# Kernel tuning notes

Hardware: AMD Instinct MI355X
Metric: run time of the kernel (lower is better)

The kernel has to match this reference:

```python
import jax, jax.numpy as jnp
import numpy as np

B, S, E, H, L, D = 16, 512, 512, 8, 3, 64
OBS, ACT, NA = 128, 16, 8
KAPPAS = jnp.asarray(1.0 - 2.0 ** (-5.0 - np.arange(H)), jnp.float32)  # per-head retention decay, decay_scaling_factor=1.0
INV_SQRT_D = 1.0 / float(np.sqrt(D))


def rmsnorm(x, w, eps=1e-6):
    return x * jax.lax.rsqrt(jnp.mean(x * x, -1, keepdims=True) + eps) * w


def swiglu(x, wg, wp):
    return jax.nn.silu(x @ wg) * (x @ wp)


def sin_pe(ts, dim):
    # sinusoidal timestep positional encoding, ts: (B,S) float -> (B,S,dim)
    half = dim // 2
    freqs = jnp.exp(-np.log(10000.0) * jnp.arange(half, dtype=jnp.float32) / half)
    ang = ts[..., None] * freqs
    return jnp.concatenate([jnp.sin(ang), jnp.cos(ang)], -1)


def retention(xk, xq, xv, h0, ts, wq, wk, wv, wo, masked):
    # chunkwise multi-scale retention with cross-chunk recurrent state h0: (B,H,D,D)
    b, s, e = xq.shape
    pe = sin_pe(ts, e)
    q = ((xq + pe) @ wq).reshape(b, s, H, D).transpose(0, 2, 1, 3)            # (B,H,S,D)
    k = ((xk + pe) @ wk).reshape(b, s, H, D).transpose(0, 2, 1, 3) * INV_SQRT_D
    v = ((xv + pe) @ wv).reshape(b, s, H, D).transpose(0, 2, 1, 3)
    lk = jnp.log(KAPPAS)                                                      # (H,)
    diff = ts[:, None, :, None] - ts[:, None, None, :]                        # (B,1,S,S) timestep gaps
    if masked:
        idx = jnp.arange(s)
        allow = (diff > 0) | ((diff == 0) & (idx[:, None] >= idx[None, :]))
        dmat = jnp.where(allow, jnp.exp(lk[None, :, None, None] * diff), 0.0)
    else:
        dmat = jnp.exp(lk[None, :, None, None] * jnp.abs(diff))
    scores = jnp.einsum('bhnd,bhmd->bhnm', q, k) * dmat                       # decay-masked scores
    xi = jnp.exp(lk[None, :, None] * (ts[:, None, :] + 1.0))                  # (B,H,S) cross-chunk decay
    out = jnp.einsum('bhnm,bhmd->bhnd', scores, v) + jnp.einsum('bhnd,bhde->bhne', q, h0) * xi[..., None]
    tmax = ts.max(-1)                                                         # (B,)
    wst = jnp.exp(lk[None, :, None] * (tmax[:, None, None] - ts[:, None, :]))  # (B,H,S)
    h_new = jnp.exp(lk[None, :] * (tmax[:, None] + 1.0))[..., None, None] * h0 \
        + jnp.einsum('bhm,bhmd,bhme->bhde', wst, k, v)
    out = out.transpose(0, 2, 1, 3).reshape(b, s, e) @ wo
    return out, h_new


def _forward(obs, action, enc_hs, dec_hs1, dec_hs2, step_count, params):
    (eoln, eow, eln, ewq, ewk, ewv, ewo, eln1, eln2, efg, efp,
     ehw1, ehb1, ehln, ehw2, ehb2,
     daw, dln, dwq1, dwk1, dwv1, dwo1, dwq2, dwk2, dwv2, dwo2,
     dln1, dln2, dln3, dfg, dfp,
     dhw1, dhb1, dhln, dhw2, dhb2) = params
    ts = step_count.astype(jnp.float32)
    # ---- Encoder ----
    obs_rep = jax.nn.gelu(rmsnorm(obs, eoln) @ eow)
    enc_new = []
    for i in range(L):
        x = rmsnorm(obs_rep, eln)
        ret, hn = retention(x, x, x, enc_hs[:, i], ts, ewq[i], ewk[i], ewv[i], ewo[i], masked=False)
        x = rmsnorm(x + ret, eln1[i])
        obs_rep = rmsnorm(x + swiglu(x, efg[i], efp[i]), eln2[i])
        enc_new.append(hn)
    value = rmsnorm(jax.nn.gelu(obs_rep @ ehw1 + ehb1), ehln) @ ehw2 + ehb2
    # ---- Decoder ----
    x = rmsnorm(jax.nn.gelu(action @ daw), dln)
    d1_new, d2_new = [], []
    for i in range(L):
        ret, h1 = retention(x, x, x, dec_hs1[:, i], ts, dwq1[i], dwk1[i], dwv1[i], dwo1[i], masked=True)
        r = rmsnorm(x + ret, dln1[i])
        ret2, h2 = retention(r, obs_rep, r, dec_hs2[:, i], ts, dwq2[i], dwk2[i], dwv2[i], dwo2[i], masked=True)
        y = rmsnorm(obs_rep + ret2, dln2[i])
        x = rmsnorm(y + swiglu(y, dfg[i], dfp[i]), dln3[i])
        d1_new.append(h1)
        d2_new.append(h2)
    logits = rmsnorm(jax.nn.gelu(x @ dhw1 + dhb1), dhln) @ dhw2 + dhb2
    return value, logits, jnp.stack(enc_new, 1), jnp.stack(d1_new, 1), jnp.stack(d2_new, 1)


def setup_inputs():
    key = jax.random.key(0)
    ki = iter(jax.random.split(key, 50))
    def w(shape, s=0.02):
        return jax.random.normal(next(ki), shape, jnp.float32) * s
    inp = {
        'obs': jax.random.normal(next(ki), (B, S, OBS), jnp.float32),
        'action': jax.random.uniform(next(ki), (B, S, ACT + 1), jnp.float32),
        'enc_hs': jnp.zeros((B, L, H, D, D), jnp.float32),
        'dec_hs1': jnp.zeros((B, L, H, D, D), jnp.float32),
        'dec_hs2': jnp.zeros((B, L, H, D, D), jnp.float32),
        'step_count': jnp.broadcast_to(jnp.arange(S, dtype=jnp.int32) // NA, (B, S)),
        'enc_obs_ln_w': jnp.ones((OBS,), jnp.float32),
        'enc_obs_w': w((OBS, E)),
        'enc_ln_w': jnp.ones((E,), jnp.float32),
        'enc_wq': w((L, E, E)), 'enc_wk': w((L, E, E)), 'enc_wv': w((L, E, E)), 'enc_wo': w((L, E, E)),
        'enc_ln1_w': jnp.ones((L, E), jnp.float32), 'enc_ln2_w': jnp.ones((L, E), jnp.float32),
        'enc_ffn_gate': w((L, E, E)), 'enc_ffn_proj': w((L, E, E)),
        'enc_head_w1': w((E, E)), 'enc_head_b1': jnp.zeros((E,), jnp.float32),
        'enc_head_ln': jnp.ones((E,), jnp.float32),
        'enc_head_w2': w((E, 1)), 'enc_head_b2': jnp.zeros((1,), jnp.float32),
        'dec_act_w': w((ACT + 1, E)), 'dec_ln_w': jnp.ones((E,), jnp.float32),
        'dec_wq1': w((L, E, E)), 'dec_wk1': w((L, E, E)), 'dec_wv1': w((L, E, E)), 'dec_wo1': w((L, E, E)),
        'dec_wq2': w((L, E, E)), 'dec_wk2': w((L, E, E)), 'dec_wv2': w((L, E, E)), 'dec_wo2': w((L, E, E)),
        'dec_ln1_w': jnp.ones((L, E), jnp.float32), 'dec_ln2_w': jnp.ones((L, E), jnp.float32),
        'dec_ln3_w': jnp.ones((L, E), jnp.float32),
        'dec_ffn_gate': w((L, E, E)), 'dec_ffn_proj': w((L, E, E)),
        'dec_head_w1': w((E, E)), 'dec_head_b1': jnp.zeros((E,), jnp.float32),
        'dec_head_ln': jnp.ones((E,), jnp.float32),
        'dec_head_w2': w((E, ACT)), 'dec_head_b2': jnp.zeros((ACT,), jnp.float32),
    }
    return inp


def reference(obs, action, enc_hs, dec_hs1, dec_hs2, step_count, enc_obs_ln_w, enc_obs_w, enc_ln_w, enc_wq, enc_wk, enc_wv, enc_wo, enc_ln1_w, enc_ln2_w, enc_ffn_gate, enc_ffn_proj, enc_head_w1, enc_head_b1, enc_head_ln, enc_head_w2, enc_head_b2, dec_act_w, dec_ln_w, dec_wq1, dec_wk1, dec_wv1, dec_wo1, dec_wq2, dec_wk2, dec_wv2, dec_wo2, dec_ln1_w, dec_ln2_w, dec_ln3_w, dec_ffn_gate, dec_ffn_proj, dec_head_w1, dec_head_b1, dec_head_ln, dec_head_w2, dec_head_b2):
    params = (enc_obs_ln_w, enc_obs_w, enc_ln_w, enc_wq, enc_wk, enc_wv, enc_wo, enc_ln1_w, enc_ln2_w, enc_ffn_gate, enc_ffn_proj, enc_head_w1, enc_head_b1, enc_head_ln, enc_head_w2, enc_head_b2, dec_act_w, dec_ln_w, dec_wq1, dec_wk1, dec_wv1, dec_wo1, dec_wq2, dec_wk2, dec_wv2, dec_wo2, dec_ln1_w, dec_ln2_w, dec_ln3_w, dec_ffn_gate, dec_ffn_proj, dec_head_w1, dec_head_b1, dec_head_ln, dec_head_w2, dec_head_b2)
    return _forward(obs, action, enc_hs, dec_hs1, dec_hs2, step_count, params)
```

## Files before the change

### kernel.cpp

```cpp
#include <hip/hip_runtime.h>
#include <hip/hip_bf16.h>
#include <math.h>

typedef __attribute__((ext_vector_type(8))) short short8;
typedef __attribute__((ext_vector_type(4))) short short4v;
typedef __attribute__((ext_vector_type(4))) float f32x4;

#define BB 16
#define SS 512
#define EE 512
#define HH 8
#define DH 64
#define LL 3
#define MM (BB*SS)
#define OBSD 128
#define ACTD 17
#define INV_SQRT_D 0.125f

#define ACT_NONE 0
#define ACT_GELU 1

#define NORM_PLAIN 0
#define NORM_ADD 1

// ... 17 lines not shown
__device__ __forceinline__ void gl16(const void* g, void* l){
  __builtin_amdgcn_global_load_lds((gas1_t)g, (las3_t)l, 16, 0, 0);
}

#define PIPE_SYNC do{ asm volatile("s_waitcnt vmcnt(0)" ::: "memory"); \
                      __builtin_amdgcn_s_barrier(); \
                      __builtin_amdgcn_sched_barrier(0); }while(0)

__global__ __launch_bounds__(256) void wtpose_kernel(
    const float* __restrict__ src, unsigned short* __restrict__ dst, int K, int Kpad)
{
  __shared__ float t[32][33];
  const int gx = blockIdx.x, gy = blockIdx.y;
  const int tx = threadIdx.x, ty = threadIdx.y;
  #pragma unroll
  for (int i = 0; i < 4; ++i){
    int k = gx*32 + ty + i*8, n = gy*32 + tx;
    t[ty+i*8][tx] = (k < K) ? src[(size_t)k*EE + n] : 0.f;
  }
  __syncthreads();
  #pragma unroll
  for (int i = 0; i < 4; ++i){
    int k = gx*32 + tx, n = gy*32 + ty + i*8;
    dst[(size_t)n*Kpad + k] = f2bs(t[tx][ty+i*8]);
  }
}

struct TP50 { const float* s[50]; unsigned short* d[50]; };
__global__ __launch_bounds__(256) void wtpose_batch_kernel(TP50 tp)
{
  __shared__ float t[32][33];
  const float* src = tp.s[blockIdx.z];
  unsigned short* dst = tp.d[blockIdx.z];
  const int gx = blockIdx.x, gy = blockIdx.y;
  const int tx = threadIdx.x, ty = threadIdx.y;
  #pragma unroll
  for (int i = 0; i < 4; ++i){
    int k = gx*32 + ty + i*8, n = gy*32 + tx;
    t[ty+i*8][tx] = src[(size_t)k*EE + n];
  }
  __syncthreads();
  #pragma unroll
  for (int i = 0; i < 4; ++i){
    int k = gx*32 + tx, n = gy*32 + ty + i*8;
    dst[(size_t)n*EE + k] = f2bs(t[tx][ty+i*8]);
  }
}

template<int MODE>
__global__ __launch_bounds__(256) void gemm128_kernel(
    const unsigned short* __restrict__ A, const unsigned short* __restrict__ Wt,
    const float* __restrict__ bias, unsigned short* __restrict__ Cb,
    int Kpad, float scale, int act, int gstart,
    unsigned short* __restrict__ qout, unsigned short* __restrict__ kout,
    unsigned short* __restrict__ vT)
{
  __shared__ unsigned short As[2][128*64];
  __shared__ unsigned short Bs[2][128*64];
  const int bm = blockIdx.y*128, bn = blockIdx.x*128;
  const int tid = threadIdx.x, lane = tid & 63, wv = tid >> 6;
  const int wr = wv >> 1, wc = wv & 1;
  const int l16 = lane & 15, quad = lane >> 4;

  f32x4 acc[4][4];
  #pragma unroll
  for (int i=0;i<4;i++)
    #pragma unroll
    for (int j=0;j<4;j++) acc[i][j]=(f32x4)(0.f);

  const int sg = lane >> 3;
  const int lg = (lane & 7) ^ sg;
  size_t aoff[4], boff[4];
  #pragma unroll
  for (int i=0;i<4;i++){
    aoff[i] = (size_t)(bm + wv*32 + i*8 + sg)*Kpad + lg*8;
    boff[i] = (size_t)(bn + wv*32 + i*8 + sg)*Kpad + lg*8;
  }
  const int swz = (l16 & 7) << 3;

  auto STAGE = [&](int buf, int t){
    const int k0 = t*64;
    #pragma unroll
    for (int i=0;i<4;i++){
      gl16(A + aoff[i] + k0, (char*)&As[buf][0] + ((wv*4+i) << 10));
      gl16(Wt + boff[i] + k0, (char*)&Bs[buf][0] + ((wv*4+i) << 10));
    }
  };
  auto COMPUTE = [&](int buf){
    short8 af[4][2], bf[4][2];
    #pragma unroll
    for (int mt=0; mt<4; ++mt)
      #pragma unroll
      for (int ks=0; ks<2; ++ks)
        af[mt][ks] = *(const short8*)&As[buf][(wr*64 + mt*16 + l16)*64 + ((ks*32 + quad*8) ^ swz)];
    #pragma unroll
    for (int nt=0; nt<4; ++nt)
      #pragma unroll
      for (int ks=0; ks<2; ++ks)
        bf[nt][ks] = *(const short8*)&Bs[buf][(wc*64 + nt*16 + l16)*64 + ((ks*32 + quad*8) ^ swz)];
    #pragma unroll
    for (int ks=0; ks<2; ++ks)
      #pragma unroll
      for (int mt=0; mt<4; ++mt)
        #pragma unroll
        for (int nt=0; nt<4; ++nt)
          acc[mt][nt] = __builtin_amdgcn_mfma_f32_16x16x32_bf16(af[mt][ks], bf[nt][ks], acc[mt][nt], 0, 0, 0);
  };

  const int NT = Kpad >> 6;
  STAGE(0, 0);
  PIPE_SYNC;
  int cur = 0;
  for (int t = 0; t < NT; ++t){
    if (t+1 < NT) STAGE(cur^1, t+1);
    COMPUTE(cur);
    if (t+1 < NT) PIPE_SYNC;
    cur ^= 1;
  }

  if (MODE == 0){
    #pragma unroll
    for (int mt=0; mt<4; ++mt){
      int rb = bm + wr*64 + mt*16 + quad*4;
      #pragma unroll
      for (int nt=0; nt<4; ++nt){
        int col = bn + wc*64 + nt*16 + l16;
        float bv = bias ? bias[col] : 0.f;
        #pragma unroll
        for (int j=0;j<4;j++){
          float v = acc[mt][nt][j]*scale + bv;
          if (act==ACT_GELU) v = gelu_f(v);
          Cb[(size_t)(rb+j)*EE + col] = f2bs(v);
        }
      }
    }
  } else {
    const int group = gstart + (bn >> 9);
    if (group <= 1){
      unsigned short* O = (group == 0) ? qout : kout;
      const float scl = (group == 1) ? INV_SQRT_D : 1.f;
      #pragma unroll
      for (int mt=0; mt<4; ++mt){
        int rb = bm + wr*64 + mt*16 + quad*4;
        #pragma unroll
        for (int nt=0; nt<4; ++nt){
          int ccol = (bn & 511) + wc*64 + nt*16 + l16;
          #pragma unroll
          for (int j=0;j<4;j++)
            O[(size_t)(rb+j)*EE + ccol] = f2bs(acc[mt][nt][j]*scl);
        }
      }
    } else {
      const int hh = ((bn & 511) >> 6) + wc;
      #pragma unroll
      for (int mt=0; mt<4; ++mt){
        int rb = bm + wr*64 + mt*16 + quad*4;
        int bloc = rb >> 9, m0 = rb & 511;
        #pragma unroll
        for (int nt=0; nt<4; ++nt){
          int ee = nt*16 + l16;
          size_t taddr = (((size_t)bloc*HH + hh)*DH + ee)*SS + m0;
          short4v pk;
          #pragma unroll
          for (int j=0;j<4;j++) pk[j] = (short)f2bs(acc[mt][nt][j]);
          *(short4v*)&vT[taddr] = pk;
        }
      }
    }
  }
}

__global__ __launch_bounds__(256) void gemm_sw_kernel(
    const unsigned short* __restrict__ A, const unsigned short* __restrict__ Wt,
    const unsigned short* __restrict__ Wt2, unsigned short* __restrict__ swo)
{
  __shared__ unsigned short As[2][128*64];
  __shared__ unsigned short Bs[2][64*64];
  __shared__ unsigned short Bs2[2][64*64];
  const int bm = blockIdx.y*128, bn = blockIdx.x*64;
  const int tid = threadIdx.x, lane = tid & 63, wv = tid >> 6;
  const int wr = wv >> 1, wc = wv & 1;
  const int l16 = lane & 15, quad = lane >> 4;

  f32x4 acc[4][2], acc2[4][2];
  #pragma unroll
  for (int i=0;i<4;i++){
    acc[i][0]=(f32x4)(0.f); acc[i][1]=(f32x4)(0.f);
    acc2[i][0]=(f32x4)(0.f); acc2[i][1]=(f32x4)(0.f);
  }

  const int sg = lane >> 3;
  const int lg = (lane & 7) ^ sg;
  size_t aoff[4], boff[2];
  #pragma unroll
  for (int i=0;i<4;i++)
    aoff[i] = (size_t)(bm + (wv*4+i)*8 + sg)*EE + lg*8;
  #pragma unroll
  for (int i=0;i<2;i++)
    boff[i] = (size_t)(bn + (wv*2+i)*8 + sg)*EE + lg*8;

  const int swz = (l16 & 7) << 3;

  auto STAGE = [&](int buf, int t){
    const int k0 = t*64;
    #pragma unroll
    for (int i=0;i<4;i++)
// ... 70 lines not shown
  if (mode == NORM_ADD){
    short8 rv = *(const short8*)&resb[base];
    #pragma unroll
    for (int e=0;e<8;++e) t[e] += bs2f((unsigned short)rv[e]);
  }
  float ss = 0.f;
  #pragma unroll
  for (int e=0;e<8;++e) ss += t[e]*t[e];
  #pragma unroll
  for (int o=32;o;o>>=1) ss += __shfl_xor(ss, o);
  float r = 1.f/sqrtf(ss/(float)EE + 1e-6f);
  float4 w0 = *(const float4*)&w[lane*8];
  float4 w1 = *(const float4*)&w[lane*8+4];
  float y[8];
  y[0]=t[0]*r*w0.x; y[1]=t[1]*r*w0.y; y[2]=t[2]*r*w0.z; y[3]=t[3]*r*w0.w;
  y[4]=t[4]*r*w1.x; y[5]=t[5]*r*w1.y; y[6]=t[6]*r*w1.z; y[7]=t[7]*r*w1.w;
  short8 pk;
  #pragma unroll
  for (int e=0;e<8;++e) pk[e] = (short)f2bs(y[e]);
  *(short8*)&o1[base] = pk;
  if (o2){
    short8 pv = *(const short8*)&peb[base];
    short8 pz;
    #pragma unroll
    for (int e=0;e<8;++e) pz[e] = (short)f2bs(y[e] + bs2f((unsigned short)pv[e]));
    *(short8*)&o2[base] = pz;
  }
}

__global__ __launch_bounds__(256) void norm_obs_kernel(
    const float* __restrict__ a, const float* __restrict__ w, unsigned short* __restrict__ o)
{
  const int row = blockIdx.x*4 + (threadIdx.x >> 6);
  const int lane = threadIdx.x & 63;
  const size_t base = (size_t)row*OBSD + lane*2;
  float2 av = *(const float2*)&a[base];
  float ss = av.x*av.x + av.y*av.y;
  #pragma unroll
  for (int off=32;off;off>>=1) ss += __shfl_xor(ss, off);
  float r = 1.f/sqrtf(ss/(float)OBSD + 1e-6f);
  float2 wv2 = *(const float2*)&w[lane*2];
  unsigned int pk = (unsigned int)f2bs(av.x*r*wv2.x) | ((unsigned int)f2bs(av.y*r*wv2.y) << 16);
  *(unsigned int*)&o[base] = pk;
}

__global__ __launch_bounds__(256) void act_embed_kernel(
    const float* __restrict__ a, unsigned short* __restrict__ o)
{
  int idx = blockIdx.x*256 + threadIdx.x;
  int row = idx >> 6, col = idx & 63;
  o[idx] = (col < ACTD) ? f2bs(a[(size_t)row*ACTD + col]) : 0;
}

__global__ __launch_bounds__(256) void wchunkscan_kernel(
    const unsigned short* __restrict__ k, const unsigned short* __restrict__ vT,
    const float* __restrict__ h0, const float* __restrict__ tmx,
    const int* __restrict__ tsi,
    unsigned short* __restrict__ wcum_lo, unsigned short* __restrict__ wcum_hi,
    float* __restrict__ hnew, int enc)
{
  __shared__ unsigned short vsh[64*72];
  __shared__ unsigned short ksh[64*72];
  const int h = blockIdx.x, b = blockIdx.y;
  const int tid = threadIdx.x, lane = tid & 63, wv = tid >> 6;
  const int quad = lane >> 4, l16 = lane & 15;
  const float lk = lkappa(h);
  const float elk = __expf(lk);
  const float etm = __expf(lk*tmx[b]);
  const size_t wbase = ((size_t)b*HH + h)*8*4096;
  const size_t hbase = (size_t)b*(LL*HH*DH*DH) + (size_t)h*(DH*DH);
  const int e0r = wv*16 + quad*4;
  const int sr = tid >> 2, sseg = (tid & 3)*16;

  f32x4 cum[4];
  #pragma unroll
  for (int dt=0; dt<4; ++dt)
    #pragma unroll
    for (int j=0;j<4;j++)
      cum[dt][j] = elk * h0[hbase + (size_t)(dt*16+l16)*64 + e0r + j];

  for (int c = 0; c < 8; ++c){
    __syncthreads();
    {
      const unsigned short* vrow = vT + (((size_t)b*HH + h)*DH + sr)*SS + c*64 + sseg;
      #pragma unroll
      for (int i = 0; i < 2; ++i)
        *(short8*)&vsh[sr*72 + sseg + i*8] = *(const short8*)(vrow + i*8);
      float els = __expf(-lk * (float)tsi[b*SS + c*64 + sr]);
      const unsigned short* krow = k + ((size_t)b*SS + c*64 + sr)*EE + h*DH + sseg;
      #pragma unroll
      for (int i = 0; i < 2; ++i){
        short8 kv = *(const short8*)(krow + i*8);
        #pragma unroll
        for (int e = 0; e < 8; ++e)
          ksh[(sseg + i*8 + e)*72 + sr] = f2bs(bs2f((unsigned short)kv[e])*els);
      }
    }
    __syncthreads();
    short8 av[2];
    #pragma unroll
    for (int ks=0; ks<2; ++ks)
      av[ks] = *(const short8*)&vsh[(wv*16 + l16)*72 + ks*32 + quad*8];
    f32x4 acc[4];
    #pragma unroll
    for (int dt=0; dt<4; ++dt) acc[dt] = (f32x4)(0.f);
    #pragma unroll
    for (int ks=0; ks<2; ++ks)
      #pragma unroll
      for (int dt=0; dt<4; ++dt){
        short8 kb = *(const short8*)&ksh[(dt*16 + l16)*72 + ks*32 + quad*8];
        acc[dt] = __builtin_amdgcn_mfma_f32_16x16x32_bf16(av[ks], kb, acc[dt], 0, 0, 0);
      }
    #pragma unroll
    for (int dt=0; dt<4; ++dt)
      #pragma unroll
      for (int j=0;j<4;j++){
        wcum_lo[wbase + (size_t)c*4096 + (size_t)(e0r+j)*64 + dt*16 + l16] = f2bs(cum[dt][j]);
        cum[dt][j] += acc[dt][j];
      }
  }
  #pragma unroll
  for (int dt=0; dt<4; ++dt)
    #pragma unroll
    for (int j=0;j<4;j++)
      hnew[hbase + (size_t)(dt*16+l16)*64 + e0r + j] = etm * cum[dt][j];

  if (enc){
    f32x4 suf[4];
    #pragma unroll
    for (int dt=0; dt<4; ++dt) suf[dt] = (f32x4)(0.f);
    for (int c = 7; c >= 0; --c){
      __syncthreads();
      {
        const unsigned short* vrow = vT + (((size_t)b*HH + h)*DH + sr)*SS + c*64 + sseg;
        #pragma unroll
        for (int i = 0; i < 2; ++i)
          *(short8*)&vsh[sr*72 + sseg + i*8] = *(const short8*)(vrow + i*8);
        float ehs = __expf(lk * (float)tsi[b*SS + c*64 + sr]);
        const unsigned short* krow = k + ((size_t)b*SS + c*64 + sr)*EE + h*DH + sseg;
        #pragma unroll
        for (int i = 0; i < 2; ++i){
          short8 kv = *(const short8*)(krow + i*8);
          #pragma unroll
          for (int e = 0; e < 8; ++e)
            ksh[(sseg + i*8 + e)*72 + sr] = f2bs(bs2f((unsigned short)kv[e])*ehs);
        }
      }
      __syncthreads();
      short8 av[2];
      #pragma unroll
      for (int ks=0; ks<2; ++ks)
        av[ks] = *(const short8*)&vsh[(wv*16 + l16)*72 + ks*32 + quad*8];
      f32x4 acc[4];
      #pragma unroll
      for (int dt=0; dt<4; ++dt) acc[dt] = (f32x4)(0.f);
      #pragma unroll
      for (int ks=0; ks<2; ++ks)
        #pragma unroll
        for (int dt=0; dt<4; ++dt){
          short8 kb = *(const short8*)&ksh[(dt*16 + l16)*72 + ks*32 + quad*8];
          acc[dt] = __builtin_amdgcn_mfma_f32_16x16x32_bf16(av[ks], kb, acc[dt], 0, 0, 0);
        }
      #pragma unroll
      for (int dt=0; dt<4; ++dt)
        #pragma unroll
        for (int j=0;j<4;j++){
          wcum_hi[wbase + (size_t)c*4096 + (size_t)(e0r+j)*64 + dt*16 + l16] = f2bs(suf[dt][j]);
          suf[dt][j] += acc[dt][j];
        }
    }
  }
}

template<int ENC>
__global__ __launch_bounds__(256) void retention2_kernel(
    const unsigned short* __restrict__ q, const unsigned short* __restrict__ k,
    const unsigned short* __restrict__ vT,
    const unsigned short* __restrict__ wlo, const unsigned short* __restrict__ whi,
    const int* __restrict__ tsi, unsigned short* __restrict__ outp)
{
  __shared__ unsigned short qsh[64*72];
  __shared__ unsigned short wsh[64*72];
  __shared__ unsigned short ksh[64*72];
  __shared__ unsigned short vsh[64*72];
  __shared__ unsigned short qsh2[ENC ? 64*72 : 2];
  __shared__ unsigned short wsh2[ENC ? 64*72 : 2];
  __shared__ float tsf[SS];
  const int b = blockIdx.z, h = blockIdx.y, t = blockIdx.x;
  const int n0 = t*64;
  const int tid = threadIdx.x, lane = tid & 63, wv = tid >> 6;
  const int quad = lane >> 4, l16 = lane & 15;
  const float lk = lkappa(h);

  for (int i = tid; i < SS; i += 256) tsf[i] = (float)tsi[b*SS + i];
  {
    const int n = tid >> 2, seg = (tid & 3)*16;
    float ts_n = (float)tsi[b*SS + n0 + n];
    float e0 = __expf(lk*ts_n);
    float e1 = ENC ? __expf(-lk*ts_n) : 0.f;
    const unsigned short* qr = q + ((size_t)b*SS + n0 + n)*EE + h*DH + seg;
    #pragma unroll
    for (int i = 0; i < 2; ++i){
      short8 v = *(const short8*)(qr + i*8);
      short8 o, o2;
      #pragma unroll
      for (int e=0;e<8;++e){
        float f = bs2f((unsigned short)v[e]);
        o[e] = (short)f2bs(f*e0);
        if (ENC) o2[e] = (short)f2bs(f*e1);
      }
      *(short8*)&qsh[n*72 + seg + i*8] = o;
      if (ENC) *(short8*)&qsh2[n*72 + seg + i*8] = o2;
    }
    const unsigned short* wr = wlo + (((size_t)b*HH + h)*8 + t)*4096 + (size_t)n*64 + seg;
    #pragma unroll
    for (int i = 0; i < 2; ++i)
      *(short8*)&wsh[n*72 + seg + i*8] = *(const short8*)(wr + i*8);
    if (ENC){
      const unsigned short* wr2 = whi + (((size_t)b*HH + h)*8 + t)*4096 + (size_t)n*64 + seg;
      #pragma unroll
      for (int i = 0; i < 2; ++i)
        *(short8*)&wsh2[n*72 + seg + i*8] = *(const short8*)(wr2 + i*8);
    }
// ... 108 lines not shown
      int nloc = rowbase + quad*4 + j;
      int n = n0 + nloc;
      float tsn = tsf[n];
      #pragma unroll
      for (int mt=0; mt<4; ++mt){
        float diff = tsn - tsm[mt];
        float p;
        if (ENC) p = (diff >= 0.f) ? sacc[mt][j] : sacc2[mt][j];
        else     p = ((diff > 0.f) || (diff == 0.f && n >= mg[mt])) ? sacc[mt][j] : 0.f;
        qsh[nloc*72 + mt*16 + l16] = f2bs(p);
      }
    }
    #pragma unroll
    for (int ks=0; ks<2; ++ks){
      short8 pa = *(const short8*)&qsh[(rowbase + l16)*72 + ks*32 + quad*8];
      #pragma unroll
      for (int et=0; et<4; ++et){
        short8 vb = *(const short8*)&vsh[(et*16 + l16)*72 + ks*32 + quad*8];
        acc_o[et] = __builtin_amdgcn_mfma_f32_16x16x32_bf16(pa, vb, acc_o[et], 0, 0, 0);
      }
    }
  }
  #pragma unroll
  for (int j=0;j<4;j++){
    size_t rbase = ((size_t)b*SS + n0 + rowbase + quad*4 + j)*EE + h*DH;
    #pragma unroll
    for (int et=0; et<4; ++et)
      outp[rbase + et*16 + l16] = f2bs(acc_o[et][j]);
  }
}

__global__ void tsmax_kernel(const int* __restrict__ tsi, float* __restrict__ tmx){
  __shared__ int red[4];
  int b = blockIdx.x, tid = threadIdx.x;
  int m = max(tsi[b*SS+tid], tsi[b*SS+256+tid]);
  #pragma unroll
  for (int o=32;o;o>>=1) m = max(m, __shfl_down(m,o));
  if ((tid&63)==0) red[tid>>6]=m;
  __syncthreads();
  if (tid==0) tmx[b] = (float)max(max(red[0],red[1]),max(red[2],red[3]));
}

__global__ void pe_kernel(const int* __restrict__ tsi, unsigned short* __restrict__ peb){
  int idx = blockIdx.x*256 + threadIdx.x;
  int row = idx >> 9, j = idx & 511;
  float ts = (float)tsi[row];
  int jj = j & 255;
  float freq = expf(-9.210340371976184f*(float)jj*(1.f/256.f));
  float ang = ts*freq;
  peb[idx] = f2bs((j < 256) ? sinf(ang) : cosf(ang));
}

__global__ __launch_bounds__(256) void value_head_kernel(
    const unsigned short* __restrict__ x, const float* __restrict__ w,
    const float* __restrict__ bias, float* __restrict__ outp)
{
  const int tid = threadIdx.x, lane = tid & 63, wv = tid >> 6;
  const int r8 = lane >> 3, seg = lane & 7;
  const int row = blockIdx.x*32 + wv*8 + r8;
  const unsigned short* xr = x + (size_t)row*EE + seg*64;
  const float* wr = w + seg*64;
  float s = 0.f;
  #pragma unroll
  for (int i = 0; i < 8; ++i){
    short8 xv = *(const short8*)(xr + i*8);
    #pragma unroll
    for (int e = 0; e < 8; ++e)
      s += bs2f((unsigned short)xv[e]) * wr[i*8 + e];
  }
  s += __shfl_xor(s, 1); s += __shfl_xor(s, 2); s += __shfl_xor(s, 4);
  if (seg == 0) outp[row] = s + bias[0];
}

__global__ __launch_bounds__(256) void logits_head_kernel(
    const unsigned short* __restrict__ x, const float* __restrict__ w,
    const float* __restrict__ bias, float* __restrict__ outp)
{
  __shared__ unsigned short xsh[16*520];
  __shared__ unsigned short wsh[16*520];
  const int tid = threadIdx.x;
  const int row0 = blockIdx.x*16;
  {
    const int r = tid >> 4, kc = (tid & 15)*32;
    const unsigned short* xr = x + (size_t)(row0 + r)*EE + kc;
    #pragma unroll
    for (int i = 0; i < 4; ++i)
      *(short8*)&xsh[r*520 + kc + i*8] = *(const short8*)(xr + i*8);
    const int j = r;
    #pragma unroll
    for (int kk = 0; kk < 32; ++kk)
      wsh[j*520 + kc + kk] = f2bs(w[(size_t)(kc + kk)*16 + j]);
  }
  __syncthreads();
  const int r = tid >> 4, j = tid & 15;
  float s = 0.f;
  for (int k = 0; k < EE; k += 8){
    short8 xv = *(const short8*)&xsh[r*520 + k];
    short8 wv = *(const short8*)&wsh[j*520 + k];
    #pragma unroll
    for (int e = 0; e < 8; ++e)
      s += bs2f((unsigned short)xv[e]) * bs2f((unsigned short)wv[e]);
  }
  outp[(size_t)(row0 + r)*16 + j] = s + bias[j];
}

extern "C" void kernel_launch(void* const* d_in, const int* in_sizes, int n_in,
                              void* d_out, int out_size, void* d_ws, size_t ws_size,
                              hipStream_t stream)
{
  const float* obs     = (const float*)d_in[0];
  const float* action  = (const float*)d_in[1];
  const float* enc_hs  = (const float*)d_in[2];
  const float* dec_hs1 = (const float*)d_in[3];
  const float* dec_hs2 = (const float*)d_in[4];
  const int*   stepc   = (const int*)d_in[5];
  const float* eoln = (const float*)d_in[6];
  const float* eow  = (const float*)d_in[7];
  const float* eln  = (const float*)d_in[8];
  const float* ewq  = (const float*)d_in[9];
  const float* ewk  = (const float*)d_in[10];
  const float* ewv  = (const float*)d_in[11];
  const float* ewo  = (const float*)d_in[12];
  const float* eln1 = (const float*)d_in[13];
  const float* eln2 = (const float*)d_in[14];
  const float* efg  = (const float*)d_in[15];
  const float* efp  = (const float*)d_in[16];
  const float* ehw1 = (const float*)d_in[17];
  const float* ehb1 = (const float*)d_in[18];
  const float* ehln = (const float*)d_in[19];
  const float* ehw2 = (const float*)d_in[20];
  const float* ehb2 = (const float*)d_in[21];
  const float* daw  = (const float*)d_in[22];
  const float* dln  = (const float*)d_in[23];
  const float* dwq1 = (const float*)d_in[24];
  const float* dwk1 = (const float*)d_in[25];
  const float* dwv1 = (const float*)d_in[26];
  const float* dwo1 = (const float*)d_in[27];
  const float* dwq2 = (const float*)d_in[28];
  const float* dwk2 = (const float*)d_in[29];
  const float* dwv2 = (const float*)d_in[30];
  const float* dwo2 = (const float*)d_in[31];
  const float* dln1 = (const float*)d_in[32];
  const float* dln2 = (const float*)d_in[33];
  const float* dln3 = (const float*)d_in[34];
  const float* dfg  = (const float*)d_in[35];
  const float* dfp  = (const float*)d_in[36];
  const float* dhw1 = (const float*)d_in[37];
  const float* dhb1 = (const float*)d_in[38];
  const float* dhln = (const float*)d_in[39];
  const float* dhw2 = (const float*)d_in[40];
  const float* dhb2 = (const float*)d_in[41];

  const size_t BUF = (size_t)MM*EE;
  float* wsf  = (float*)d_ws;
  float* f32a = wsf;
  float* f32b = f32a + BUF;
// ... 23 lines not shown
  if (ws_size < need) return;

  unsigned short* wt_eqkv  = wts + 0*W55;
  unsigned short* wt_ewo   = wts + 9*W55;
  unsigned short* wt_efg   = wts + 12*W55;
  unsigned short* wt_efp   = wts + 15*W55;
  unsigned short* wt_ehw1  = wts + 18*W55;
  unsigned short* wt_dqkv1 = wts + 19*W55;
  unsigned short* wt_dwo1  = wts + 28*W55;
  unsigned short* wt_dkv2  = wts + 31*W55;
  unsigned short* wt_dwq2  = wts + 37*W55;
  unsigned short* wt_dwo2  = wts + 40*W55;
  unsigned short* wt_dfg   = wts + 43*W55;
  unsigned short* wt_dfp   = wts + 46*W55;
  unsigned short* wt_dhw1  = wts + 49*W55;

  float* out        = (float*)d_out;
  float* value_out  = out;
  float* logits_out = out + 8192;
  float* enc_out    = logits_out + (size_t)MM*16;
  float* d1_out     = enc_out + (size_t)BB*LL*HH*DH*DH;
  float* d2_out     = d1_out  + (size_t)BB*LL*HH*DH*DH;

  const size_t HS_L = (size_t)HH*DH*DH;

  {
    TP50 tp;
    int z = 0;
    auto add = [&](const float* p){ tp.s[z] = p; tp.d[z] = wts + (size_t)z*W55; ++z; };
    for (int i=0;i<3;++i){ add(ewq+i*W55); add(ewk+i*W55); add(ewv+i*W55); }
    for (int i=0;i<3;++i) add(ewo+i*W55);
    for (int i=0;i<3;++i) add(efg+i*W55);
    for (int i=0;i<3;++i) add(efp+i*W55);
    add(ehw1);
    for (int i=0;i<3;++i){ add(dwq1+i*W55); add(dwk1+i*W55); add(dwv1+i*W55); }
    for (int i=0;i<3;++i) add(dwo1+i*W55);
    for (int i=0;i<3;++i){ add(dwk2+i*W55); add(dwv2+i*W55); }
    for (int i=0;i<3;++i) add(dwq2+i*W55);
    for (int i=0;i<3;++i) add(dwo2+i*W55);
    for (int i=0;i<3;++i) add(dfg+i*W55);
    for (int i=0;i<3;++i) add(dfp+i*W55);
    add(dhw1);
    wtpose_batch_kernel<<<dim3(16,16,50), dim3(32,8), 0, stream>>>(tp);
  }
  wtpose_kernel<<<dim3(4,16), dim3(32,8), 0, stream>>>(eow, wt_eow, OBSD, OBSD);
  wtpose_kernel<<<dim3(2,16), dim3(32,8), 0, stream>>>(daw, wt_daw, ACTD, 64);

  pe_kernel<<<(MM*EE)/256, 256, 0, stream>>>(stepc, peb);
  tsmax_kernel<<<BB, 256, 0, stream>>>(stepc, tmx);

  auto gemmF = [&](const unsigned short* A, const unsigned short* Wt, const float* bias,
                   unsigned short* Cb, int Kpad, float scale, int act){
    gemm128_kernel<0><<<dim3(EE/128, MM/128), 256, 0, stream>>>(A, Wt, bias, Cb,
        Kpad, scale, act, 0, nullptr, nullptr, nullptr);
  };
  auto gemmQKV = [&](const unsigned short* A, const unsigned short* Wt){
    gemm128_kernel<1><<<dim3(12, MM/128), 256, 0, stream>>>(A, Wt, nullptr, nullptr,
        EE, 1.f, ACT_NONE, 0, q_b, k_b, vT_b);
  };
  auto gemmKV = [&](const unsigned short* A, const unsigned short* Wt){
    gemm128_kernel<1><<<dim3(8, MM/128), 256, 0, stream>>>(A, Wt, nullptr, nullptr,
        EE, 1.f, ACT_NONE, 1, nullptr, k_b, vT_b);
  };
  auto gemmQ2 = [&](const unsigned short* A, const unsigned short* Wt){
    gemm128_kernel<1><<<dim3(4, MM/128), 256, 0, stream>>>(A, Wt, nullptr, nullptr,
        EE, 1.f, ACT_NONE, 0, q_b, nullptr, nullptr);
  };
  auto gemmSW = [&](const unsigned short* A, const unsigned short* Wg, const unsigned short* Wp){
    gemm_sw_kernel<<<dim3(EE/64, MM/128), 256, 0, stream>>>(A, Wg, Wp, sw_b);
  };
  auto norm = [&](const unsigned short* ab, const unsigned short* resb, const float* w,
                  unsigned short* o1, unsigned short* o2, int mode){
    norm_b_kernel<<<MM/4, 256, 0, stream>>>(ab, resb, w, o1, o2, peb, mode);
  };
  auto retention = [&](const float* h0, float* hnew, unsigned short* o, int enc){
    wchunkscan_kernel<<<dim3(HH, BB), 256, 0, stream>>>(k_b, vT_b,
        h0, tmx, stepc, wcum_lo, enc ? wcum_hi : wcum_lo, hnew, enc);
    if (enc)
      retention2_kernel<1><<<dim3(8, HH, BB), 256, 0, stream>>>(
          q_b, k_b, vT_b, wcum_lo, wcum_hi, stepc, o);
    else
      retention2_kernel<0><<<dim3(8, HH, BB), 256, 0, stream>>>(
          q_b, k_b, vT_b, wcum_lo, nullptr, stepc, o);
  };

  norm_obs_kernel<<<MM/4, 256, 0, stream>>>(obs, eoln, obs_n);
  gemmF(obs_n, wt_eow, nullptr, gf_b, OBSD, 1.f, ACT_GELU);

  for (int i = 0; i < LL; ++i){
    if (i == 0) norm(gf_b, nullptr, eln, x_b, x_pe_b, NORM_PLAIN);
    else        norm(xrep_b, nullptr, eln, x_b, x_pe_b, NORM_PLAIN);
    gemmQKV(x_pe_b, wt_eqkv + (size_t)3*i*W55);
    retention(enc_hs + i*HS_L, enc_out + i*HS_L, t1_b, 1);
    gemmF(t1_b, wt_ewo + i*W55, nullptr, gf_b, EE, 1.f, ACT_NONE);
    norm(x_b, gf_b, eln1 + i*EE, t1_b, nullptr, NORM_ADD);
    gemmSW(t1_b, wt_efg + i*W55, wt_efp + i*W55);
    norm(t1_b, sw_b, eln2 + i*EE, xrep_b, xrep_pe_b, NORM_ADD);
  }

  gemmF(xrep_b, wt_ehw1, ehb1, gf_b, EE, 1.f, ACT_GELU);
  norm(gf_b, nullptr, ehln, t1_b, nullptr, NORM_PLAIN);
  value_head_kernel<<<MM/32, 256, 0, stream>>>(t1_b, ehw2, ehb2, value_out);

  act_embed_kernel<<<(MM*64)/256, 256, 0, stream>>>(action, act_b);
  gemmF(act_b, wt_daw, nullptr, gf_b, 64, 1.f, ACT_GELU);
  norm(gf_b, nullptr, dln, x_b, x_pe_b, NORM_PLAIN);

  for (int i = 0; i < LL; ++i){
    gemmQKV(x_pe_b, wt_dqkv1 + (size_t)3*i*W55);
    retention(dec_hs1 + i*HS_L, d1_out + i*HS_L, t1_b, 0);
    gemmF(t1_b, wt_dwo1 + i*W55, nullptr, gf_b, EE, 1.f, ACT_NONE);
    norm(x_b, gf_b, dln1 + i*EE, t1_b, t1_pe_b, NORM_ADD);
    gemmQ2(xrep_pe_b, wt_dwq2 + i*W55);
    gemmKV(t1_pe_b, wt_dkv2 + (size_t)2*i*W55);
    retention(dec_hs2 + i*HS_L, d2_out + i*HS_L, t1_b, 0);
    gemmF(t1_b, wt_dwo2 + i*W55, nullptr, gf_b, EE, 1.f, ACT_NONE);
    norm(xrep_b, gf_b, dln2 + i*EE, x_b, nullptr, NORM_ADD);
    gemmSW(x_b, wt_dfg + i*W55, wt_dfp + i*W55);
    norm(x_b, sw_b, dln3 + i*EE, x_b, x_pe_b, NORM_ADD);
  }

  gemmF(x_b, wt_dhw1, dhb1, gf_b, EE, 1.f, ACT_GELU);
  norm(gf_b, nullptr, dhln, t1_b, nullptr, NORM_PLAIN);
  logits_head_kernel<<<MM/16, 256, 0, stream>>>(t1_b, dhw2, dhb2, logits_out);
}
```

Measured before the change: 1.169 ms.

## Split chunk scan across D halves and passes, fuse heads and cross-attn GEMMs

The chunk-scan kernel is split over the two halves of the key dimension, and in the encoder the forward and backward passes run as separate blocks. Its chunk loads are double-buffered, so the grid grows from 128 to 256 or 512 blocks. The decoder's Q2 and KV2 projections are merged into one GEMM launch via a split point on the column block index. The final RMSNorm is folded into the value and logits head kernels, removing a norm launch and an intermediate round trip each. The trade-off is more kernel complexity and extra per-block setup, with duplicated V loads across the D halves.

```diff
diff --git a/kernel.cpp b/kernel.cpp
--- a/kernel.cpp
+++ b/kernel.cpp
@@ -93,6 +93,8 @@
     const unsigned short* __restrict__ A, const unsigned short* __restrict__ Wt,
     const float* __restrict__ bias, unsigned short* __restrict__ Cb,
     int Kpad, float scale, int act, int gstart,
+    const unsigned short* __restrict__ A2, const unsigned short* __restrict__ Wt2,
+    int split_bn, int g2,
     unsigned short* __restrict__ qout, unsigned short* __restrict__ kout,
     unsigned short* __restrict__ vT)
 {
@@ -103,6 +105,15 @@
   const int wr = wv >> 1, wc = wv & 1;
   const int l16 = lane & 15, quad = lane >> 4;
 
+  const unsigned short* Ap = A;
+  const unsigned short* Wp = Wt;
+  int bnl = bn;
+  int group = 0;
+  if (MODE == 1){
+    if (bn >= split_bn){ Ap = A2; Wp = Wt2; bnl = bn - split_bn; group = g2 + (bnl >> 9); }
+    else group = gstart + (bnl >> 9);
+  }
+
   f32x4 acc[4][4];
   #pragma unroll
   for (int i=0;i<4;i++)
@@ -115,7 +126,7 @@
   #pragma unroll
   for (int i=0;i<4;i++){
     aoff[i] = (size_t)(bm + wv*32 + i*8 + sg)*Kpad + lg*8;
-    boff[i] = (size_t)(bn + wv*32 + i*8 + sg)*Kpad + lg*8;
+    boff[i] = (size_t)(bnl + wv*32 + i*8 + sg)*Kpad + lg*8;
   }
   const int swz = (l16 & 7) << 3;
 
@@ -123,8 +134,8 @@
     const int k0 = t*64;
     #pragma unroll
     for (int i=0;i<4;i++){
-      gl16(A + aoff[i] + k0, (char*)&As[buf][0] + ((wv*4+i) << 10));
-      gl16(Wt + boff[i] + k0, (char*)&Bs[buf][0] + ((wv*4+i) << 10));
+      gl16(Ap + aoff[i] + k0, (char*)&As[buf][0] + ((wv*4+i) << 10));
+      gl16(Wp + boff[i] + k0, (char*)&Bs[buf][0] + ((wv*4+i) << 10));
     }
   };
   auto COMPUTE = [&](int buf){
@@ -176,7 +187,6 @@
       }
     }
   } else {
-    const int group = gstart + (bn >> 9);
     if (group <= 1){
       unsigned short* O = (group == 0) ? qout : kout;
       const float scl = (group == 1) ? INV_SQRT_D : 1.f;
@@ -185,14 +195,14 @@
         int rb = bm + wr*64 + mt*16 + quad*4;
         #pragma unroll
         for (int nt=0; nt<4; ++nt){
-          int ccol = (bn & 511) + wc*64 + nt*16 + l16;
+          int ccol = (bnl & 511) + wc*64 + nt*16 + l16;
           #pragma unroll
           for (int j=0;j<4;j++)
             O[(size_t)(rb+j)*EE + ccol] = f2bs(acc[mt][nt][j]*scl);
         }
       }
     } else {
-      const int hh = ((bn & 511) >> 6) + wc;
+      const int hh = ((bnl & 511) >> 6) + wc;
       #pragma unroll
       for (int mt=0; mt<4; ++mt){
         int rb = bm + wr*64 + mt*16 + quad*4;
@@ -369,16 +379,19 @@
   o[idx] = (col < ACTD) ? f2bs(a[(size_t)row*ACTD + col]) : 0;
 }
 
+template<int ENC>
 __global__ __launch_bounds__(256) void wchunkscan_kernel(
     const unsigned short* __restrict__ k, const unsigned short* __restrict__ vT,
     const float* __restrict__ h0, const float* __restrict__ tmx,
     const int* __restrict__ tsi,
     unsigned short* __restrict__ wcum_lo, unsigned short* __restrict__ wcum_hi,
-    float* __restrict__ hnew, int enc)
-{
-  __shared__ unsigned short vsh[64*72];
-  __shared__ unsigned short ksh[64*72];
-  const int h = blockIdx.x, b = blockIdx.y;
+    float* __restrict__ hnew)
+{
+  __shared__ unsigned short vsh[2][64*72];
+  __shared__ unsigned short ksh[2][32*72];
+  const int gx = blockIdx.x, h = blockIdx.y, b = blockIdx.z;
+  const int dhalf = gx & 1;
+  const int pass = ENC ? (gx >> 1) : 0;
   const int tid = threadIdx.x, lane = tid & 63, wv = tid >> 6;
   const int quad = lane >> 4, l16 = lane & 15;
   const float lk = lkappa(h);
@@ -387,105 +400,81 @@
   const size_t wbase = ((size_t)b*HH + h)*8*4096;
   const size_t hbase = (size_t)b*(LL*HH*DH*DH) + (size_t)h*(DH*DH);
   const int e0r = wv*16 + quad*4;
-  const int sr = tid >> 2, sseg = (tid & 3)*16;
-
-  f32x4 cum[4];
-  #pragma unroll
-  for (int dt=0; dt<4; ++dt)
+  const int rv = tid >> 2, segv = (tid & 3)*16;
+  const int kact = ((tid & 3) < 2), segk = (tid & 1)*16;
+  const int rk = tid >> 2;
+  const float ksgn = pass ? lk : -lk;
+  unsigned short* wout = pass ? wcum_hi : wcum_lo;
+  const int c0 = pass ? 7 : 0, dc = pass ? -1 : 1;
+
+  f32x4 cum[2];
+  #pragma unroll
+  for (int dt=0; dt<2; ++dt)
     #pragma unroll
     for (int j=0;j<4;j++)
-      cum[dt][j] = elk * h0[hbase + (size_t)(dt*16+l16)*64 + e0r + j];
-
-  for (int c = 0; c < 8; ++c){
-    __syncthreads();
-    {
-      const unsigned short* vrow = vT + (((size_t)b*HH + h)*DH + sr)*SS + c*64 + sseg;
-      #pragma unroll
-      for (int i = 0; i < 2; ++i)
-        *(short8*)&vsh[sr*72 + sseg + i*8] = *(const short8*)(vrow + i*8);
-      float els = __expf(-lk * (float)tsi[b*SS + c*64 + sr]);
-      const unsigned short* krow = k + ((size_t)b*SS + c*64 + sr)*EE + h*DH + sseg;
-      #pragma unroll
-      for (int i = 0; i < 2; ++i){
-        short8 kv = *(const short8*)(krow + i*8);
-        #pragma unroll
-        for (int e = 0; e < 8; ++e)
-          ksh[(sseg + i*8 + e)*72 + sr] = f2bs(bs2f((unsigned short)kv[e])*els);
-      }
-    }
-    __syncthreads();
-    short8 av[2];
-    #pragma unroll
-    for (int ks=0; ks<2; ++ks)
-      av[ks] = *(const short8*)&vsh[(wv*16 + l16)*72 + ks*32 + quad*8];
-    f32x4 acc[4];
-    #pragma unroll
-    for (int dt=0; dt<4; ++dt) acc[dt] = (f32x4)(0.f);
-    #pragma unroll
-    for (int ks=0; ks<2; ++ks)
-      #pragma unroll
-      for (int dt=0; dt<4; ++dt){
-        short8 kb = *(const short8*)&ksh[(dt*16 + l16)*72 + ks*32 + quad*8];
-        acc[dt] = __builtin_amdgcn_mfma_f32_16x16x32_bf16(av[ks], kb, acc[dt], 0, 0, 0);
-      }
-    #pragma unroll
-    for (int dt=0; dt<4; ++dt)
+      cum[dt][j] = pass ? 0.f
+        : elk * h0[hbase + (size_t)(dhalf*32 + dt*16 + l16)*64 + e0r + j];
+
+  short8 vv0, vv1, kv0, kv1;
+  float kts = 0.f;
+  auto LOADR = [&](int c){
+    const unsigned short* vrow = vT + (((size_t)b*HH + h)*DH + rv)*SS + c*64 + segv;
+    vv0 = *(const short8*)(vrow);
+    vv1 = *(const short8*)(vrow + 8);
+    if (kact){
+      const unsigned short* krow = k + ((size_t)b*SS + c*64 + rk)*EE + h*DH + dhalf*32 + segk;
+      kv0 = *(const short8*)(krow);
+      kv1 = *(const short8*)(krow + 8);
+      kts = (float)tsi[b*SS + c*64 + rk];
+    }
+  };
+  auto WRITE = [&](int buf){
+    *(short8*)&vsh[buf][rv*72 + segv] = vv0;
+    *(short8*)&vsh[buf][rv*72 + segv + 8] = vv1;
+    if (kact){
+      float els = __expf(ksgn*kts);
+      #pragma unroll
+      for (int e=0;e<8;++e){
+        ksh[buf][(segk + e)*72 + rk]     = f2bs(bs2f((unsigned short)kv0[e])*els);
+        ksh[buf][(segk + 8 + e)*72 + rk] = f2bs(bs2f((unsigned short)kv1[e])*els);
+      }
+    }
+  };
+
+  LOADR(c0);
+  WRITE(0);
+  __syncthreads();
+  int cur = 0;
+  for (int i=0;i<8;++i){
+    const int c = c0 + dc*i;
+    if (i<7) LOADR(c + dc);
+    short8 av0 = *(const short8*)&vsh[cur][(wv*16 + l16)*72 + quad*8];
+    short8 av1 = *(const short8*)&vsh[cur][(wv*16 + l16)*72 + 32 + quad*8];
+    f32x4 acc[2];
+    #pragma unroll
+    for (int dt=0; dt<2; ++dt){
+      f32x4 a = (f32x4)(0.f);
+      short8 kb0 = *(const short8*)&ksh[cur][(dt*16 + l16)*72 + quad*8];
+      short8 kb1 = *(const short8*)&ksh[cur][(dt*16 + l16)*72 + 32 + quad*8];
+      a = __builtin_amdgcn_mfma_f32_16x16x32_bf16(av0, kb0, a, 0, 0, 0);
+      a = __builtin_amdgcn_mfma_f32_16x16x32_bf16(av1, kb1, a, 0, 0, 0);
+      acc[dt] = a;
+    }
+    #pragma unroll
+    for (int dt=0; dt<2; ++dt)
       #pragma unroll
       for (int j=0;j<4;j++){
-        wcum_lo[wbase + (size_t)c*4096 + (size_t)(e0r+j)*64 + dt*16 + l16] = f2bs(cum[dt][j]);
+        wout[wbase + (size_t)c*4096 + (size_t)(e0r+j)*64 + dhalf*32 + dt*16 + l16] = f2bs(cum[dt][j]);
         cum[dt][j] += acc[dt][j];
       }
-  }
-  #pragma unroll
-  for (int dt=0; dt<4; ++dt)
-    #pragma unroll
-    for (int j=0;j<4;j++)
-      hnew[hbase + (size_t)(dt*16+l16)*64 + e0r + j] = etm * cum[dt][j];
-
-  if (enc){
-    f32x4 suf[4];
-    #pragma unroll
-    for (int dt=0; dt<4; ++dt) suf[dt] = (f32x4)(0.f);
-    for (int c = 7; c >= 0; --c){
-      __syncthreads();
-      {
-        const unsigned short* vrow = vT + (((size_t)b*HH + h)*DH + sr)*SS + c*64 + sseg;
-        #pragma unroll
-        for (int i = 0; i < 2; ++i)
-          *(short8*)&vsh[sr*72 + sseg + i*8] = *(const short8*)(vrow + i*8);
-        float ehs = __expf(lk * (float)tsi[b*SS + c*64 + sr]);
-        const unsigned short* krow = k + ((size_t)b*SS + c*64 + sr)*EE + h*DH + sseg;
-        #pragma unroll
-        for (int i = 0; i < 2; ++i){
-          short8 kv = *(const short8*)(krow + i*8);
-          #pragma unroll
-          for (int e = 0; e < 8; ++e)
-            ksh[(sseg + i*8 + e)*72 + sr] = f2bs(bs2f((unsigned short)kv[e])*ehs);
-        }
-      }
-      __syncthreads();
-      short8 av[2];
-      #pragma unroll
-      for (int ks=0; ks<2; ++ks)
-        av[ks] = *(const short8*)&vsh[(wv*16 + l16)*72 + ks*32 + quad*8];
-      f32x4 acc[4];
-      #pragma unroll
-      for (int dt=0; dt<4; ++dt) acc[dt] = (f32x4)(0.f);
-      #pragma unroll
-      for (int ks=0; ks<2; ++ks)
-        #pragma unroll
-        for (int dt=0; dt<4; ++dt){
-          short8 kb = *(const short8*)&ksh[(dt*16 + l16)*72 + ks*32 + quad*8];
-          acc[dt] = __builtin_amdgcn_mfma_f32_16x16x32_bf16(av[ks], kb, acc[dt], 0, 0, 0);
-        }
-      #pragma unroll
-      for (int dt=0; dt<4; ++dt)
-        #pragma unroll
-        for (int j=0;j<4;j++){
-          wcum_hi[wbase + (size_t)c*4096 + (size_t)(e0r+j)*64 + dt*16 + l16] = f2bs(suf[dt][j]);
-          suf[dt][j] += acc[dt][j];
-        }
-    }
+    if (i<7){ WRITE(cur^1); __syncthreads(); cur ^= 1; }
+  }
+  if (!pass){
+    #pragma unroll
+    for (int dt=0; dt<2; ++dt)
+      #pragma unroll
+      for (int j=0;j<4;j++)
+        hnew[hbase + (size_t)(dhalf*32 + dt*16 + l16)*64 + e0r + j] = etm * cum[dt][j];
   }
 }
 
@@ -700,56 +689,83 @@
 }
 
 __global__ __launch_bounds__(256) void value_head_kernel(
-    const unsigned short* __restrict__ x, const float* __restrict__ w,
-    const float* __restrict__ bias, float* __restrict__ outp)
-{
-  const int tid = threadIdx.x, lane = tid & 63, wv = tid >> 6;
-  const int r8 = lane >> 3, seg = lane & 7;
-  const int row = blockIdx.x*32 + wv*8 + r8;
-  const unsigned short* xr = x + (size_t)row*EE + seg*64;
-  const float* wr = w + seg*64;
-  float s = 0.f;
-  #pragma unroll
-  for (int i = 0; i < 8; ++i){
-    short8 xv = *(const short8*)(xr + i*8);
-    #pragma unroll
-    for (int e = 0; e < 8; ++e)
-      s += bs2f((unsigned short)xv[e]) * wr[i*8 + e];
-  }
-  s += __shfl_xor(s, 1); s += __shfl_xor(s, 2); s += __shfl_xor(s, 4);
-  if (seg == 0) outp[row] = s + bias[0];
+    const unsigned short* __restrict__ x, const float* __restrict__ ln,
+    const float* __restrict__ w, const float* __restrict__ bias,
+    float* __restrict__ outp)
+{
+  const int row = blockIdx.x*4 + (threadIdx.x >> 6);
+  const int lane = threadIdx.x & 63;
+  const size_t base = (size_t)row*EE + lane*8;
+  short8 xv = *(const short8*)&x[base];
+  float4 l0 = *(const float4*)&ln[lane*8];
+  float4 l1 = *(const float4*)&ln[lane*8+4];
+  float4 w0 = *(const float4*)&w[lane*8];
+  float4 w1 = *(const float4*)&w[lane*8+4];
+  float lw[8] = {l0.x*w0.x, l0.y*w0.y, l0.z*w0.z, l0.w*w0.w,
+                 l1.x*w1.x, l1.y*w1.y, l1.z*w1.z, l1.w*w1.w};
+  float ss = 0.f, dp = 0.f;
+  #pragma unroll
+  for (int e=0;e<8;++e){
+    float f = bs2f((unsigned short)xv[e]);
+    ss += f*f;
+    dp += f*lw[e];
+  }
+  #pragma unroll
+  for (int o=32;o;o>>=1){ ss += __shfl_xor(ss,o); dp += __shfl_xor(dp,o); }
+  if (lane==0) outp[row] = dp*(1.f/sqrtf(ss/(float)EE + 1e-6f)) + bias[0];
 }
 
 __global__ __launch_bounds__(256) void logits_head_kernel(
-    const unsigned short* __restrict__ x, const float* __restrict__ w,
-    const float* __restrict__ bias, float* __restrict__ outp)
-{
-  __shared__ unsigned short xsh[16*520];
+    const unsigned short* __restrict__ x, const float* __restrict__ ln,
+    const float* __restrict__ w, const float* __restrict__ bias,
+    float* __restrict__ outp)
+{
+  __shared__ unsigned short ysh[16*528];
   __shared__ unsigned short wsh[16*520];
   const int tid = threadIdx.x;
   const int row0 = blockIdx.x*16;
+  const int g = tid >> 4, j16 = tid & 15;
   {
-    const int r = tid >> 4, kc = (tid & 15)*32;
-    const unsigned short* xr = x + (size_t)(row0 + r)*EE + kc;
-    #pragma unroll
-    for (int i = 0; i < 4; ++i)
-      *(short8*)&xsh[r*520 + kc + i*8] = *(const short8*)(xr + i*8);
-    const int j = r;
+    const int kc = j16*32;
     #pragma unroll
     for (int kk = 0; kk < 32; ++kk)
-      wsh[j*520 + kc + kk] = f2bs(w[(size_t)(kc + kk)*16 + j]);
+      wsh[g*520 + kc + kk] = f2bs(w[(size_t)(kc + kk)*16 + g]);
+  }
+  {
+    const unsigned short* xr = x + (size_t)(row0+g)*EE + j16*32;
+    float xs[32];
+    float ss = 0.f;
+    #pragma unroll
+    for (int i=0;i<4;++i){
+      short8 v = *(const short8*)(xr + i*8);
+      #pragma unroll
+      for (int e=0;e<8;++e){ float f = bs2f((unsigned short)v[e]); xs[i*8+e]=f; ss += f*f; }
+    }
+    ss += __shfl_xor(ss,1); ss += __shfl_xor(ss,2);
+    ss += __shfl_xor(ss,4); ss += __shfl_xor(ss,8);
+    float r = 1.f/sqrtf(ss/(float)EE + 1e-6f);
+    #pragma unroll
+    for (int i=0;i<4;++i){
+      float4 la = *(const float4*)&ln[j16*32 + i*8];
+      float4 lb = *(const float4*)&ln[j16*32 + i*8 + 4];
+      short8 o;
+      o[0]=(short)f2bs(xs[i*8+0]*r*la.x); o[1]=(short)f2bs(xs[i*8+1]*r*la.y);
+      o[2]=(short)f2bs(xs[i*8+2]*r*la.z); o[3]=(short)f2bs(xs[i*8+3]*r*la.w);
+      o[4]=(short)f2bs(xs[i*8+4]*r*lb.x); o[5]=(short)f2bs(xs[i*8+5]*r*lb.y);
+      o[6]=(short)f2bs(xs[i*8+6]*r*lb.z); o[7]=(short)f2bs(xs[i*8+7]*r*lb.w);
+      *(short8*)&ysh[g*528 + j16*32 + i*8] = o;
+    }
   }
   __syncthreads();
-  const int r = tid >> 4, j = tid & 15;
   float s = 0.f;
-  for (int k = 0; k < EE; k += 8){
-    short8 xv = *(const short8*)&xsh[r*520 + k];
-    short8 wv = *(const short8*)&wsh[j*520 + k];
+  for (int kk = 0; kk < EE; kk += 8){
+    short8 xv = *(const short8*)&ysh[g*528 + kk];
+    short8 wv = *(const short8*)&wsh[j16*520 + kk];
     #pragma unroll
     for (int e = 0; e < 8; ++e)
       s += bs2f((unsigned short)xv[e]) * bs2f((unsigned short)wv[e]);
   }
-  outp[(size_t)(row0 + r)*16 + j] = s + bias[j];
+  outp[(size_t)(row0 + g)*16 + j16] = s + bias[j16];
 }
 
 extern "C" void kernel_launch(void* const* d_in, const int* in_sizes, int n_in,
@@ -879,19 +895,16 @@
   auto gemmF = [&](const unsigned short* A, const unsigned short* Wt, const float* bias,
                    unsigned short* Cb, int Kpad, float scale, int act){
     gemm128_kernel<0><<<dim3(EE/128, MM/128), 256, 0, stream>>>(A, Wt, bias, Cb,
-        Kpad, scale, act, 0, nullptr, nullptr, nullptr);
+        Kpad, scale, act, 0, nullptr, nullptr, 1<<30, 0, nullptr, nullptr, nullptr);
   };
   auto gemmQKV = [&](const unsigned short* A, const unsigned short* Wt){
     gemm128_kernel<1><<<dim3(12, MM/128), 256, 0, stream>>>(A, Wt, nullptr, nullptr,
-        EE, 1.f, ACT_NONE, 0, q_b, k_b, vT_b);
-  };
-  auto gemmKV = [&](const unsigned short* A, const unsigned short* Wt){
-    gemm128_kernel<1><<<dim3(8, MM/128), 256, 0, stream>>>(A, Wt, nullptr, nullptr,
-        EE, 1.f, ACT_NONE, 1, nullptr, k_b, vT_b);
-  };
-  auto gemmQ2 = [&](const unsigned short* A, const unsigned short* Wt){
-    gemm128_kernel<1><<<dim3(4, MM/128), 256, 0, stream>>>(A, Wt, nullptr, nullptr,
-        EE, 1.f, ACT_NONE, 0, q_b, nullptr, nullptr);
+        EE, 1.f, ACT_NONE, 0, nullptr, nullptr, 1<<30, 0, q_b, k_b, vT_b);
+  };
+  auto gemmQ2KV = [&](const unsigned short* A1, const unsigned short* Wq2,
+                      const unsigned short* A2, const unsigned short* Wkv2){
+    gemm128_kernel<1><<<dim3(12, MM/128), 256, 0, stream>>>(A1, Wq2, nullptr, nullptr,
+        EE, 1.f, ACT_NONE, 0, A2, Wkv2, 512, 1, q_b, k_b, vT_b);
   };
   auto gemmSW = [&](const unsigned short* A, const unsigned short* Wg, const unsigned short* Wp){
     gemm_sw_kernel<<<dim3(EE/64, MM/128), 256, 0, stream>>>(A, Wg, Wp, sw_b);
@@ -901,14 +914,17 @@
     norm_b_kernel<<<MM/4, 256, 0, stream>>>(ab, resb, w, o1, o2, peb, mode);
   };
   auto retention = [&](const float* h0, float* hnew, unsigned short* o, int enc){
-    wchunkscan_kernel<<<dim3(HH, BB), 256, 0, stream>>>(k_b, vT_b,
-        h0, tmx, stepc, wcum_lo, enc ? wcum_hi : wcum_lo, hnew, enc);
-    if (enc)
+    if (enc){
+      wchunkscan_kernel<1><<<dim3(4, HH, BB), 256, 0, stream>>>(k_b, vT_b,
+          h0, tmx, stepc, wcum_lo, wcum_hi, hnew);
       retention2_kernel<1><<<dim3(8, HH, BB), 256, 0, stream>>>(
           q_b, k_b, vT_b, wcum_lo, wcum_hi, stepc, o);
-    else
+    } else {
+      wchunkscan_kernel<0><<<dim3(2, HH, BB), 256, 0, stream>>>(k_b, vT_b,
+          h0, tmx, stepc, wcum_lo, nullptr, hnew);
       retention2_kernel<0><<<dim3(8, HH, BB), 256, 0, stream>>>(
           q_b, k_b, vT_b, wcum_lo, nullptr, stepc, o);
+    }
   };
 
   norm_obs_kernel<<<MM/4, 256, 0, stream>>>(obs, eoln, obs_n);
@@ -926,8 +942,7 @@
   }
 
   gemmF(xrep_b, wt_ehw1, ehb1, gf_b, EE, 1.f, ACT_GELU);
-  norm(gf_b, nullptr, ehln, t1_b, nullptr, NORM_PLAIN);
-  value_head_kernel<<<MM/32, 256, 0, stream>>>(t1_b, ehw2, ehb2, value_out);
+  value_head_kernel<<<MM/4, 256, 0, stream>>>(gf_b, ehln, ehw2, ehb2, value_out);
 
   act_embed_kernel<<<(MM*64)/256, 256, 0, stream>>>(action, act_b);
   gemmF(act_b, wt_daw, nullptr, gf_b, 64, 1.f, ACT_GELU);
@@ -938,8 +953,7 @@
     retention(dec_hs1 + i*HS_L, d1_out + i*HS_L, t1_b, 0);
     gemmF(t1_b, wt_dwo1 + i*W55, nullptr, gf_b, EE, 1.f, ACT_NONE);
     norm(x_b, gf_b, dln1 + i*EE, t1_b, t1_pe_b, NORM_ADD);
-    gemmQ2(xrep_pe_b, wt_dwq2 + i*W55);
-    gemmKV(t1_pe_b, wt_dkv2 + (size_t)2*i*W55);
+    gemmQ2KV(xrep_pe_b, wt_dwq2 + i*W55, t1_pe_b, wt_dkv2 + (size_t)2*i*W55);
     retention(dec_hs2 + i*HS_L, d2_out + i*HS_L, t1_b, 0);
     gemmF(t1_b, wt_dwo2 + i*W55, nullptr, gf_b, EE, 1.f, ACT_NONE);
     norm(xrep_b, gf_b, dln2 + i*EE, x_b, nullptr, NORM_ADD);
@@ -948,6 +962,5 @@
   }
 
   gemmF(x_b, wt_dhw1, dhb1, gf_b, EE, 1.f, ACT_GELU);
-  norm(gf_b, nullptr, dhln, t1_b, nullptr, NORM_PLAIN);
-  logits_head_kernel<<<MM/16, 256, 0, stream>>>(t1_b, dhw2, dhb2, logits_out);
-}
+  logits_head_kernel<<<MM/16, 256, 0, stream>>>(gf_b, dhln, dhw2, dhb2, logits_out);
+}
```

Result: faster. 1.137 ms (-2.7%).
